# Performance work log

Measured on AMD Instinct MI355X. Metric: run time of the kernel, lower is better.

## Reference

```python
import jax, jax.numpy as jnp
import numpy as np

KERNEL_MUL = 2.0
KERNEL_NUM = 5


def _index_matrix(b: int) -> jnp.ndarray:
    # non-linear JMMD index matrix (linear=False)
    im = np.zeros((2 * b, 2 * b), dtype=np.float32)
    off = 1.0 / float(b * (b - 1))
    eye = np.eye(b, dtype=bool)
    im[:b, :b][~eye] = off
    im[b:, b:][~eye] = off
    im[:b, b:] = -1.0 / float(b * b)
    im[b:, :b] = -1.0 / float(b * b)
    return jnp.asarray(im)


def _gaussian_kernel(source, target):
    total = jnp.concatenate([source, target], axis=0)  # [2b, d]
    n = total.shape[0]
    sq = jnp.sum(total * total, axis=1)  # [2b]
    # pairwise squared L2 via Gram matrix (same math as expand/diff/sum)
    l2 = sq[:, None] + sq[None, :] - 2.0 * (total @ total.T)
    l2 = jnp.maximum(l2, 0.0)
    # bandwidth computed on detached distances (torch uses .data)
    bw = jax.lax.stop_gradient(jnp.sum(l2)) / float(n * n - n)
    bw = bw / (KERNEL_MUL ** (KERNEL_NUM // 2))
    k = jnp.zeros_like(l2)
    for i in range(KERNEL_NUM):
        k = k + jnp.exp(-l2 / (bw * (KERNEL_MUL ** i)))
    return k


def setup_inputs() -> dict:
    key = jax.random.key(0)
    k1, k2, k3, k4 = jax.random.split(key, 4)
    b, d1, d2 = 2048, 4096, 2048
    return {
        "z1_s": jax.random.normal(k1, (b, d1), dtype=jnp.float32),
        "z1_t": jax.random.normal(k2, (b, d1), dtype=jnp.float32),
        "z2_s": jax.random.normal(k3, (b, d2), dtype=jnp.float32),
        "z2_t": jax.random.normal(k4, (b, d2), dtype=jnp.float32),
    }


def reference(z1_s, z1_t, z2_s, z2_t):
    b = z1_s.shape[0]
    index_matrix = _index_matrix(b)  # [2b, 2b]
    kernel_matrix = _gaussian_kernel(z1_s, z1_t) * _gaussian_kernel(z2_s, z2_t)
    loss = jnp.sum(kernel_matrix * index_matrix) + 2.0 / float(b - 1)
    return loss
```

## Files before the change

kernel.cpp:

```cpp
#include <hip/hip_runtime.h>
#include <cstdint>

#define NTOT 4096
#define BHALF 2048
#define D1 4096
#define D2 2048
#define TT 32
#define NTILES 528

typedef __attribute__((ext_vector_type(4))) float f32x4;
typedef __attribute__((ext_vector_type(8))) int i32x8;

__device__ __forceinline__ void glds16(const uint8_t* g, uint8_t* l) {
    __builtin_amdgcn_global_load_lds(
        (const __attribute__((address_space(1))) void*)(uintptr_t)g,
        (__attribute__((address_space(3))) void*)(uint32_t)(uintptr_t)l,
        16, 0, 0);
}

__device__ __forceinline__ float fp8dec(unsigned b) {
    unsigned e = (b >> 3) & 15u, m = b & 7u;
    float v = e ? __uint_as_float(((e + 120u) << 23) | (m << 20))
                : (float)m * 0.001953125f;
    return (b & 128u) ? -v : v;
}

__global__ void prep_kernel(const float* __restrict__ z1s, const float* __restrict__ z1t,
                            const float* __restrict__ z2s, const float* __restrict__ z2t,
                            float* __restrict__ sq1, float* __restrict__ sq2,
                            uint8_t* __restrict__ t1f8, uint8_t* __restrict__ t2f8,
                            float* __restrict__ s1, float* __restrict__ s2) {
    int bid = blockIdx.x;
    int tid = threadIdx.x;
    if (bid == 0) { for (int i = tid; i < 4096; i += 256) s1[i] = 0.f; }
    if (bid == 1) { for (int i = tid; i < 2048; i += 256) s2[i] = 0.f; }
    int which = bid >> 12;
    int row = bid & 4095;
    int d = which ? D2 : D1;
    const float* s_ = which ? z2s : z1s;
    const float* t_ = which ? z2t : z1t;
    const float* src = (row < BHALF) ? s_ + (size_t)row * d : t_ + (size_t)(row - BHALF) * d;
    uint8_t* dst = (which ? t2f8 : t1f8) + (size_t)row * d;
    float* sq = which ? sq2 : sq1;
    const float4* src4 = (const float4*)src;
    float a = 0.f;
    int n8 = d >> 3;
    for (int i = tid; i < n8; i += 256) {
        float4 v0 = src4[2 * i], v1 = src4[2 * i + 1];
        a += v0.x * v0.x + v0.y * v0.y + v0.z * v0.z + v0.w * v0.w;
        a += v1.x * v1.x + v1.y * v1.y + v1.z * v1.z + v1.w * v1.w;
        int w0 = __builtin_amdgcn_cvt_pk_fp8_f32(v0.x, v0.y, 0, 0);
        w0 = __builtin_amdgcn_cvt_pk_fp8_f32(v0.z, v0.w, w0, 1);
        int w1 = __builtin_amdgcn_cvt_pk_fp8_f32(v1.x, v1.y, 0, 0);
        w1 = __builtin_amdgcn_cvt_pk_fp8_f32(v1.z, v1.w, w1, 1);
        ((uint2*)dst)[i] = uint2{(unsigned)w0, (unsigned)w1};
    }
    for (int o = 32; o; o >>= 1) a += __shfl_down(a, o);
    __shared__ float sh[4];
    int lane = tid & 63, w = tid >> 6;
    if (lane == 0) sh[w] = a;
    __syncthreads();
    if (tid == 0) sq[row] = sh[0] + sh[1] + sh[2] + sh[3];
}

__global__ void colsum_fp8_kernel(const uint8_t* __restrict__ t1f8,
                                  const uint8_t* __restrict__ t2f8,
                                  float* __restrict__ s1, float* __restrict__ s2) {
    int bid = blockIdx.x;
    int which = bid >= 256;
    int local = which ? bid - 256 : bid;
    int d = which ? D2 : D1;
    int colchunks = d >> 10;
    int cb = local % colchunks, rb = local / colchunks;
    const uint8_t* base = which ? t2f8 : t1f8;
    float* s = which ? s2 : s1;
    int col = (cb << 10) + threadIdx.x * 4;
    int r0 = rb * 64;
    float a0 = 0.f, a1 = 0.f, a2 = 0.f, a3 = 0.f;
    const uint8_t* p = base + (size_t)r0 * d + col;
#pragma unroll 4
    for (int r = 0; r < 64; ++r) {
        uchar4 u = *(const uchar4*)(p + (size_t)r * d);
        a0 += fp8dec(u.x); a1 += fp8dec(u.y); a2 += fp8dec(u.z); a3 += fp8dec(u.w);
    }
    atomicAdd(&s[col], a0); atomicAdd(&s[col + 1], a1);
    atomicAdd(&s[col + 2], a2); atomicAdd(&s[col + 3], a3);
}

__global__ void finalize_kernel(const float* __restrict__ s1, const float* __restrict__ s2,
                                const float* __restrict__ sq1, const float* __restrict__ sq2,
                                float* __restrict__ acc, float* __restrict__ out) {
    int tid = threadIdx.x;
    float a1 = 0.f, a2 = 0.f, q1 = 0.f, q2 = 0.f;
    for (int i = tid; i < 4096; i += 256) { float v = s1[i]; a1 += v * v; q1 += sq1[i]; q2 += sq2[i]; }
    for (int i = tid; i < 2048; i += 256) { float v = s2[i]; a2 += v * v; }
    for (int o = 32; o; o >>= 1) {
        a1 += __shfl_down(a1, o); a2 += __shfl_down(a2, o);
        q1 += __shfl_down(q1, o); q2 += __shfl_down(q2, o);
    }
    __shared__ float sh[4][4];
    int lane = tid & 63, w = tid >> 6;
    if (lane == 0) { sh[0][w] = a1; sh[1][w] = a2; sh[2][w] = q1; sh[3][w] = q2; }
    __syncthreads();
    if (tid == 0) {
        double ss1 = (double)sh[0][0] + sh[0][1] + sh[0][2] + sh[0][3];
        double ss2 = (double)sh[1][0] + sh[1][1] + sh[1][2] + sh[1][3];
        double t1 = (double)sh[2][0] + sh[2][1] + sh[2][2] + sh[2][3];
        double t2 = (double)sh[3][0] + sh[3][1] + sh[3][2] + sh[3][3];
        double S1 = 2.0 * (double)NTOT * t1 - 2.0 * ss1;
        double S2 = 2.0 * (double)NTOT * t2 - 2.0 * ss2;
        const double L2E = 1.4426950408889634;
        double nn = (double)NTOT * (double)(NTOT - 1);
        acc[2] = (float)(nn * L2E / (4.0 * S1));
        acc[3] = (float)(nn * L2E / (4.0 * S2));
        out[0] = 2.0f / (float)(BHALF - 1);
    }
}

__device__ __forceinline__ void gemm_loop_mx(const uint8_t* __restrict__ ga,
                                             const uint8_t* __restrict__ gb,
                                             int d, uint8_t* As, uint8_t* Bs,
                                             f32x4 (&acc)[4][4], int wv, int lane,
                                             int wm, int wn, int lm, int quad) {
    int rsub = lane >> 3;
    int ch = lane & 7;
    const uint8_t* gaL = ga + (size_t)(wv * 32 + rsub) * d + ch * 16;
    const uint8_t* gbL = gb + (size_t)(wv * 32 + rsub) * d + ch * 16;
    uint8_t* AsW = As + wv * 32 * 128;
    uint8_t* BsW = Bs + wv * 32 * 128;
    for (int k0 = 0; k0 < d; k0 += 128) {
        __syncthreads();
#pragma unroll
        for (int i = 0; i < 4; ++i) {
            glds16(gaL + ((size_t)i * 8 * d + k0), AsW + i * 8 * 128);
            glds16(gbL + ((size_t)i * 8 * d + k0), BsW + i * 8 * 128);
        }
        __syncthreads();
        union F { uint4 h[2]; i32x8 v; };
        F a[4];
#pragma unroll
        for (int mi = 0; mi < 4; ++mi) {
            const uint4* p = (const uint4*)&As[(wm * 64 + mi * 16 + lm) * 128 + quad * 32];
            a[mi].h[0] = p[0]; a[mi].h[1] = p[1];
        }
#pragma unroll
        for (int ni = 0; ni < 4; ++ni) {
            F b;
            const uint4* p = (const uint4*)&Bs[(wn * 64 + ni * 16 + lm) * 128 + quad * 32];
            b.h[0] = p[0]; b.h[1] = p[1];
#pragma unroll
            for (int mi = 0; mi < 4; ++mi)
                acc[mi][ni] = __builtin_amdgcn_mfma_scale_f32_16x16x128_f8f6f4(
                    a[mi].v, b.v, acc[mi][ni], 0, 0, 0, 0x7F7F7F7F, 0, 0x7F7F7F7F);
        }
    }
}

__global__ __launch_bounds__(256, 4) void gram_kernel(
    const uint8_t* __restrict__ t1f8, const uint8_t* __restrict__ t2f8,
    float* __restrict__ G1, float* __restrict__ G2) {
    __shared__ alignas(16) uint8_t As[128 * 128];
    __shared__ alignas(16) uint8_t Bs[128 * 128];
    int lid = blockIdx.x;
    int lin = (lid & 7) * 132 + (lid >> 3);
    int ti, tj, which;
    if (lin < 768) {
        int r = lin >> 7, q = lin & 127;
        which = q & 1;
        int t = q >> 1, a = t >> 3, b = t & 7;
        const int si_t[6] = {0, 0, 0, 1, 1, 2};
        const int sj_t[6] = {1, 2, 3, 2, 3, 3};
        ti = si_t[r] * 8 + a; tj = sj_t[r] * 8 + b;
    } else {
        int m = lin - 768;
        int dd = m / 144, q = m % 144;
        which = q & 1;
        int t = q >> 1;
        int s = 2 * dd + (t >= 36 ? 1 : 0);
        int tl = t >= 36 ? t - 36 : t;
        int a = 0;
        while (tl >= 8 - a) { tl -= 8 - a; ++a; }
        ti = s * 8 + a; tj = s * 8 + a + tl;
    }
    int tcan = TT * ti - (ti * (ti - 1)) / 2 + (tj - ti);
    int i0 = ti * 128, j0 = tj * 128;
    int d = which ? D2 : D1;
    const uint8_t* base = which ? t2f8 : t1f8;
    float* G = (which ? G2 : G1) + (size_t)tcan * 16384;

    int tid = threadIdx.x, lane = tid & 63, wv = tid >> 6;
    int wm = wv >> 1, wn = wv & 1, lm = lane & 15, quad = lane >> 4;
    f32x4 acc[4][4] = {};
    gemm_loop_mx(base + (size_t)i0 * d, base + (size_t)j0 * d, d, As, Bs, acc,
                 wv, lane, wm, wn, lm, quad);
#pragma unroll
    for (int mi = 0; mi < 4; ++mi)
#pragma unroll
        for (int ni = 0; ni < 4; ++ni)
#pragma unroll
            for (int rr = 0; rr < 4; ++rr)
                G[(size_t)(wm * 64 + mi * 16 + quad * 4 + rr) * 128 + wn * 64 + ni * 16 + lm] =
                    acc[mi][ni][rr];
}

__global__ __launch_bounds__(256, 4) void epi_kernel(
    const float* __restrict__ G1, const float* __restrict__ G2,
    const float* __restrict__ sq1, const float* __restrict__ sq2,
    const float* __restrict__ cv, float* __restrict__ out) {
    __shared__ float sqi1[128], sqj1[128], sqi2[128], sqj2[128];
    __shared__ float red[4];
    int t = blockIdx.x;
    int ti = 0, r = t;
    while (r >= TT - ti) { r -= TT - ti; ++ti; }
    int tj = ti + r;
    int i0 = ti * 128, j0 = tj * 128;
    int tid = threadIdx.x;
    if (tid < 128) {
        sqi1[tid] = sq1[i0 + tid]; sqj1[tid] = sq1[j0 + tid];
        sqi2[tid] = sq2[i0 + tid]; sqj2[tid] = sq2[j0 + tid];
    }
    __syncthreads();
    float c1 = cv[0], c2 = cv[1];
    const float4* g1 = (const float4*)(G1 + (size_t)t * 16384);
    const float4* g2 = (const float4*)(G2 + (size_t)t * 16384);
    bool diag = (ti == tj);
    float local = 0.f;
#pragma unroll 4
    for (int it = 0; it < 16; ++it) {
        int e4 = it * 256 + tid;
        int row = e4 >> 5, col = (e4 & 31) * 4;
        float4 a = g1[e4], b = g2[e4];
        float si1 = sqi1[row], si2 = sqi2[row];
        float ax[4] = {a.x, a.y, a.z, a.w}, bx[4] = {b.x, b.y, b.z, b.w};
#pragma unroll
        for (int j = 0; j < 4; ++j) {
            float l2a = fmaxf(si1 + sqj1[col + j] - 2.f * ax[j], 0.f);
            float l2b = fmaxf(si2 + sqj2[col + j] - 2.f * bx[j], 0.f);
            float t1 = __builtin_amdgcn_exp2f(-l2a * c1);
            float k1 = t1; float u1 = t1 * t1; k1 += u1; u1 *= u1; k1 += u1; u1 *= u1; k1 += u1; u1 *= u1; k1 += u1;
            float t2 = __builtin_amdgcn_exp2f(-l2b * c2);
            float k2 = t2; float u2 = t2 * t2; k2 += u2; u2 *= u2; k2 += u2; u2 *= u2; k2 += u2; u2 *= u2; k2 += u2;
            float v = k1 * k2;
            if (diag && (row == col + j)) v = 0.f;
            local += v;
        }
    }
    for (int o = 32; o; o >>= 1) local += __shfl_down(local, o);
    int lane = tid & 63, wv = tid >> 6;
    if (lane == 0) red[wv] = local;
    __syncthreads();
    if (tid == 0) {
        bool same = (i0 < BHALF) == (j0 < BHALF);
        float w = same ? (1.0f / ((float)BHALF * (float)(BHALF - 1)))
                       : (-1.0f / ((float)BHALF * (float)BHALF));
        if (!diag) w *= 2.f;
        atomicAdd(out, (red[0] + red[1] + red[2] + red[3]) * w);
    }
}

__global__ __launch_bounds__(256, 2) void jmmd_fused(
    const uint8_t* __restrict__ t1f8, const uint8_t* __restrict__ t2f8,
    const float* __restrict__ sq1, const float* __restrict__ sq2,
    const float* __restrict__ cv, float* __restrict__ out) {
    __shared__ alignas(16) uint8_t As[128 * 128];
    __shared__ alignas(16) uint8_t Bs[128 * 128];
    __shared__ float sqi1[128], sqj1[128], sqi2[128], sqj2[128];
    __shared__ float red[4];
    int tid = threadIdx.x;
    int ti = 0, r = blockIdx.x;
    while (r >= TT - ti) { r -= TT - ti; ++ti; }
    int tj = ti + r;
    int i0 = ti * 128, j0 = tj * 128;
    if (tid < 128) {
        sqi1[tid] = sq1[i0 + tid]; sqj1[tid] = sq1[j0 + tid];
        sqi2[tid] = sq2[i0 + tid]; sqj2[tid] = sq2[j0 + tid];
    }
    int lane = tid & 63, wv = tid >> 6;
    int wm = wv >> 1, wn = wv & 1, lm = lane & 15, quad = lane >> 4;
    f32x4 acc1[4][4] = {};
    f32x4 acc2[4][4] = {};
    gemm_loop_mx(t1f8 + (size_t)i0 * D1, t1f8 + (size_t)j0 * D1, D1, As, Bs, acc1, wv, lane, wm, wn, lm, quad);
    gemm_loop_mx(t2f8 + (size_t)i0 * D2, t2f8 + (size_t)j0 * D2, D2, As, Bs, acc2, wv, lane, wm, wn, lm, quad);
    float c1 = cv[0], c2 = cv[1];
    float local = 0.f;
    bool diag = (ti == tj);
#pragma unroll
    for (int mi = 0; mi < 4; ++mi) {
        int rbase = wm * 64 + mi * 16 + quad * 4;
#pragma unroll
        for (int ni = 0; ni < 4; ++ni) {
            int col = wn * 64 + ni * 16 + lm;
            float sb1 = sqj1[col], sb2 = sqj2[col];
#pragma unroll
            for (int rr = 0; rr < 4; ++rr) {
                int row = rbase + rr;
                float l2a = fmaxf(sqi1[row] + sb1 - 2.f * acc1[mi][ni][rr], 0.f);
                float l2b = fmaxf(sqi2[row] + sb2 - 2.f * acc2[mi][ni][rr], 0.f);
                float t1 = __builtin_amdgcn_exp2f(-l2a * c1);
                float k1 = t1; float u1 = t1 * t1; k1 += u1; u1 *= u1; k1 += u1; u1 *= u1; k1 += u1; u1 *= u1; k1 += u1;
                float t2 = __builtin_amdgcn_exp2f(-l2b * c2);
                float k2 = t2; float u2 = t2 * t2; k2 += u2; u2 *= u2; k2 += u2; u2 *= u2; k2 += u2; u2 *= u2; k2 += u2;
                float v = k1 * k2;
                if (diag && (row == col)) v = 0.f;
                local += v;
            }
        }
    }
    for (int o = 32; o; o >>= 1) local += __shfl_down(local, o);
    if (lane == 0) red[wv] = local;
    __syncthreads();
    if (tid == 0) {
        bool same = (i0 < BHALF) == (j0 < BHALF);
        float w = same ? (1.0f / ((float)BHALF * (float)(BHALF - 1)))
                       : (-1.0f / ((float)BHALF * (float)BHALF));
        if (!diag) w *= 2.f;
        atomicAdd(out, (red[0] + red[1] + red[2] + red[3]) * w);
    }
}

extern "C" void kernel_launch(void* const* d_in, const int* in_sizes, int n_in,
                              void* d_out, int out_size, void* d_ws, size_t ws_size,
                              hipStream_t stream) {
    const float* z1s = (const float*)d_in[0];
    const float* z1t = (const float*)d_in[1];
    const float* z2s = (const float*)d_in[2];
    const float* z2t = (const float*)d_in[3];
    float* out = (float*)d_out;

    float* ws = (float*)d_ws;
    float* sq1 = ws;
    float* sq2 = ws + 4096;
    float* s1  = ws + 8192;
    float* s2  = ws + 12288;
    float* acc = ws + 14336;
    uint8_t* t1f8 = (uint8_t*)(ws + 14344);
    uint8_t* t2f8 = t1f8 + (size_t)NTOT * D1;
    float* G1 = (float*)(t2f8 + (size_t)NTOT * D2);
    float* G2 = G1 + (size_t)NTILES * 16384;
    size_t need_big = (size_t)14344 * 4
                    + ((size_t)NTOT * D1 + (size_t)NTOT * D2)
                    + (size_t)NTILES * 16384 * 2 * 4;

    prep_kernel<<<8192, 256, 0, stream>>>(z1s, z1t, z2s, z2t, sq1, sq2, t1f8, t2f8, s1, s2);
    colsum_fp8_kernel<<<384, 256, 0, stream>>>(t1f8, t2f8, s1, s2);
    finalize_kernel<<<1, 256, 0, stream>>>(s1, s2, sq1, sq2, acc, out);

    if (ws_size >= need_big) {
        gram_kernel<<<1056, 256, 0, stream>>>(t1f8, t2f8, G1, G2);
        epi_kernel<<<NTILES, 256, 0, stream>>>(G1, G2, sq1, sq2, acc + 2, out);
    } else {
        jmmd_fused<<<NTILES, 256, 0, stream>>>(t1f8, t2f8, sq1, sq2, acc + 2, out);
    }
}
```

Before: 302.8 us.

## Double-buffer FP8 GEMM tiles in LDS with XOR swizzle and manual waitcnt

Replaces the single-buffered GEMM loop with a two-stage pipeline. The next K-slice is prefetched into a second LDS buffer via global_load_lds while MFMAs run on the current one, with explicit vmcnt waits and raw barriers. LDS rows are XOR-swizzled on write and on the ds_read_b128 reads to avoid bank conflicts. LDS per block doubles to 64KB, so gram_kernel's occupancy hint drops to two blocks per CU. The loop also issues a redundant wrap-around prefetch on its last step.

```diff
diff --git a/kernel.cpp b/kernel.cpp
--- a/kernel.cpp
+++ b/kernel.cpp
@@ -9,6 +9,7 @@
 #define NTILES 528
 
 typedef __attribute__((ext_vector_type(4))) float f32x4;
+typedef __attribute__((ext_vector_type(4))) int i32x4;
 typedef __attribute__((ext_vector_type(8))) int i32x8;
 
 __device__ __forceinline__ void glds16(const uint8_t* g, uint8_t* l) {
@@ -16,6 +17,12 @@
         (const __attribute__((address_space(1))) void*)(uintptr_t)g,
         (__attribute__((address_space(3))) void*)(uint32_t)(uintptr_t)l,
         16, 0, 0);
+}
+
+__device__ __forceinline__ i32x4 ldsr(uint32_t addr) {
+    i32x4 r;
+    asm volatile("ds_read_b128 %0, %1" : "=v"(r) : "v"(addr));
+    return r;
 }
 
 __device__ __forceinline__ float fp8dec(unsigned b) {
@@ -117,50 +124,79 @@
     }
 }
 
-__device__ __forceinline__ void gemm_loop_mx(const uint8_t* __restrict__ ga,
+__device__ __forceinline__ void gemm_mx_pipe(const uint8_t* __restrict__ ga,
                                              const uint8_t* __restrict__ gb,
-                                             int d, uint8_t* As, uint8_t* Bs,
+                                             int d,
+                                             uint8_t* A0, uint8_t* B0,
+                                             uint8_t* A1, uint8_t* B1,
                                              f32x4 (&acc)[4][4], int wv, int lane,
                                              int wm, int wn, int lm, int quad) {
+    int nsteps = d >> 7;
     int rsub = lane >> 3;
-    int ch = lane & 7;
-    const uint8_t* gaL = ga + (size_t)(wv * 32 + rsub) * d + ch * 16;
-    const uint8_t* gbL = gb + (size_t)(wv * 32 + rsub) * d + ch * 16;
-    uint8_t* AsW = As + wv * 32 * 128;
-    uint8_t* BsW = Bs + wv * 32 * 128;
-    for (int k0 = 0; k0 < d; k0 += 128) {
-        __syncthreads();
+    int ql = (lane & 7) ^ rsub;
+    const uint8_t* pa = ga + (size_t)(wv * 32 + rsub) * d + ql * 16;
+    const uint8_t* pb = gb + (size_t)(wv * 32 + rsub) * d + ql * 16;
+    uint8_t* dA[2] = { A0 + wv * 4096, A1 + wv * 4096 };
+    uint8_t* dB[2] = { B0 + wv * 4096, B1 + wv * 4096 };
+    uint32_t baseA[2] = { (uint32_t)(uintptr_t)A0, (uint32_t)(uintptr_t)A1 };
+    uint32_t baseB[2] = { (uint32_t)(uintptr_t)B0, (uint32_t)(uintptr_t)B1 };
+    int s0 = ((2 * quad) ^ (lm & 7)) * 16;
+    int s1 = ((2 * quad + 1) ^ (lm & 7)) * 16;
+    uint32_t offA[4], offB[4];
+#pragma unroll
+    for (int i = 0; i < 4; ++i) {
+        offA[i] = (uint32_t)((wm * 64 + i * 16 + lm) * 128);
+        offB[i] = (uint32_t)((wn * 64 + i * 16 + lm) * 128);
+    }
+#pragma unroll
+    for (int i = 0; i < 4; ++i) {
+        glds16(pa + (size_t)i * 8 * d, dA[0] + i * 1024);
+        glds16(pb + (size_t)i * 8 * d, dB[0] + i * 1024);
+    }
+    for (int k = 0; k < nsteps; ++k) {
+        int cur = k & 1, nxt = cur ^ 1;
+        size_t koff = (size_t)((k + 1 < nsteps) ? (k + 1) : 0) << 7;
 #pragma unroll
         for (int i = 0; i < 4; ++i) {
-            glds16(gaL + ((size_t)i * 8 * d + k0), AsW + i * 8 * 128);
-            glds16(gbL + ((size_t)i * 8 * d + k0), BsW + i * 8 * 128);
+            glds16(pa + koff + (size_t)i * 8 * d, dA[nxt] + i * 1024);
+            glds16(pb + koff + (size_t)i * 8 * d, dB[nxt] + i * 1024);
         }
-        __syncthreads();
-        union F { uint4 h[2]; i32x8 v; };
-        F a[4];
-#pragma unroll
-        for (int mi = 0; mi < 4; ++mi) {
-            const uint4* p = (const uint4*)&As[(wm * 64 + mi * 16 + lm) * 128 + quad * 32];
-            a[mi].h[0] = p[0]; a[mi].h[1] = p[1];
-        }
-#pragma unroll
-        for (int ni = 0; ni < 4; ++ni) {
-            F b;
-            const uint4* p = (const uint4*)&Bs[(wn * 64 + ni * 16 + lm) * 128 + quad * 32];
-            b.h[0] = p[0]; b.h[1] = p[1];
+        asm volatile("s_waitcnt vmcnt(8)\n\ts_barrier" ::: "memory");
+        i32x4 a00, a01, a10, a11, a20, a21, a30, a31;
+        i32x4 b00, b01, b10, b11, b20, b21, b30, b31;
+        a00 = ldsr(baseA[cur] + offA[0] + s0); a01 = ldsr(baseA[cur] + offA[0] + s1);
+        a10 = ldsr(baseA[cur] + offA[1] + s0); a11 = ldsr(baseA[cur] + offA[1] + s1);
+        a20 = ldsr(baseA[cur] + offA[2] + s0); a21 = ldsr(baseA[cur] + offA[2] + s1);
+        a30 = ldsr(baseA[cur] + offA[3] + s0); a31 = ldsr(baseA[cur] + offA[3] + s1);
+        b00 = ldsr(baseB[cur] + offB[0] + s0); b01 = ldsr(baseB[cur] + offB[0] + s1);
+        b10 = ldsr(baseB[cur] + offB[1] + s0); b11 = ldsr(baseB[cur] + offB[1] + s1);
+        b20 = ldsr(baseB[cur] + offB[2] + s0); b21 = ldsr(baseB[cur] + offB[2] + s1);
+        b30 = ldsr(baseB[cur] + offB[3] + s0); b31 = ldsr(baseB[cur] + offB[3] + s1);
+        asm volatile("s_waitcnt lgkmcnt(0)"
+                     : "+v"(a00), "+v"(a01), "+v"(a10), "+v"(a11),
+                       "+v"(a20), "+v"(a21), "+v"(a30), "+v"(a31),
+                       "+v"(b00), "+v"(b01), "+v"(b10), "+v"(b11),
+                       "+v"(b20), "+v"(b21), "+v"(b30), "+v"(b31));
+        union F { i32x4 h[2]; i32x8 v; };
+        F ua[4], ub[4];
+        ua[0].h[0] = a00; ua[0].h[1] = a01; ua[1].h[0] = a10; ua[1].h[1] = a11;
+        ua[2].h[0] = a20; ua[2].h[1] = a21; ua[3].h[0] = a30; ua[3].h[1] = a31;
+        ub[0].h[0] = b00; ub[0].h[1] = b01; ub[1].h[0] = b10; ub[1].h[1] = b11;
+        ub[2].h[0] = b20; ub[2].h[1] = b21; ub[3].h[0] = b30; ub[3].h[1] = b31;
+#pragma unroll
+        for (int ni = 0; ni < 4; ++ni)
 #pragma unroll
             for (int mi = 0; mi < 4; ++mi)
                 acc[mi][ni] = __builtin_amdgcn_mfma_scale_f32_16x16x128_f8f6f4(
-                    a[mi].v, b.v, acc[mi][ni], 0, 0, 0, 0x7F7F7F7F, 0, 0x7F7F7F7F);
-        }
-    }
-}
-
-__global__ __launch_bounds__(256, 4) void gram_kernel(
+                    ua[mi].v, ub[ni].v, acc[mi][ni], 0, 0, 0, 0x7F7F7F7F, 0, 0x7F7F7F7F);
+        asm volatile("s_barrier" ::: "memory");
+    }
+}
+
+__global__ __launch_bounds__(256, 2) void gram_kernel(
     const uint8_t* __restrict__ t1f8, const uint8_t* __restrict__ t2f8,
     float* __restrict__ G1, float* __restrict__ G2) {
-    __shared__ alignas(16) uint8_t As[128 * 128];
-    __shared__ alignas(16) uint8_t Bs[128 * 128];
+    __shared__ alignas(16) uint8_t smem[4][16384];
     int lid = blockIdx.x;
     int lin = (lid & 7) * 132 + (lid >> 3);
     int ti, tj, which;
@@ -191,8 +227,9 @@
     int tid = threadIdx.x, lane = tid & 63, wv = tid >> 6;
     int wm = wv >> 1, wn = wv & 1, lm = lane & 15, quad = lane >> 4;
     f32x4 acc[4][4] = {};
-    gemm_loop_mx(base + (size_t)i0 * d, base + (size_t)j0 * d, d, As, Bs, acc,
-                 wv, lane, wm, wn, lm, quad);
+    gemm_mx_pipe(base + (size_t)i0 * d, base + (size_t)j0 * d, d,
+                 smem[0], smem[1], smem[2], smem[3],
+                 acc, wv, lane, wm, wn, lm, quad);
 #pragma unroll
     for (int mi = 0; mi < 4; ++mi)
 #pragma unroll
@@ -262,8 +299,7 @@
     const uint8_t* __restrict__ t1f8, const uint8_t* __restrict__ t2f8,
     const float* __restrict__ sq1, const float* __restrict__ sq2,
     const float* __restrict__ cv, float* __restrict__ out) {
-    __shared__ alignas(16) uint8_t As[128 * 128];
-    __shared__ alignas(16) uint8_t Bs[128 * 128];
+    __shared__ alignas(16) uint8_t smem[4][16384];
     __shared__ float sqi1[128], sqj1[128], sqi2[128], sqj2[128];
     __shared__ float red[4];
     int tid = threadIdx.x;
@@ -279,8 +315,11 @@
     int wm = wv >> 1, wn = wv & 1, lm = lane & 15, quad = lane >> 4;
     f32x4 acc1[4][4] = {};
     f32x4 acc2[4][4] = {};
-    gemm_loop_mx(t1f8 + (size_t)i0 * D1, t1f8 + (size_t)j0 * D1, D1, As, Bs, acc1, wv, lane, wm, wn, lm, quad);
-    gemm_loop_mx(t2f8 + (size_t)i0 * D2, t2f8 + (size_t)j0 * D2, D2, As, Bs, acc2, wv, lane, wm, wn, lm, quad);
+    gemm_mx_pipe(t1f8 + (size_t)i0 * D1, t1f8 + (size_t)j0 * D1, D1,
+                 smem[0], smem[1], smem[2], smem[3], acc1, wv, lane, wm, wn, lm, quad);
+    asm volatile("s_waitcnt vmcnt(0)\n\ts_barrier" ::: "memory");
+    gemm_mx_pipe(t2f8 + (size_t)i0 * D2, t2f8 + (size_t)j0 * D2, D2,
+                 smem[0], smem[1], smem[2], smem[3], acc2, wv, lane, wm, wn, lm, quad);
     float c1 = cv[0], c2 = cv[1];
     float local = 0.f;
     bool diag = (ti == tj);
```

Result: faster. 294.4 us (-2.8%).
